# Kernel tuning notes

Hardware: AMD Instinct MI355X
Metric: run time of the kernel (lower is better)

The kernel has to match this reference:

```python
import jax, jax.numpy as jnp
import numpy as np

N_NODES = 100000
N_EDGES = 1600000
N_GRAPHS = 1000
D_IN = 128
HID = 128
OUT = 6


def setup_inputs() -> dict:
    key = jax.random.key(0)
    ks = jax.random.split(key, 12)
    s = 1.0 / np.sqrt(HID)
    x = jax.random.normal(ks[0], (N_NODES, D_IN), dtype=jnp.float32)
    ei = jax.random.randint(ks[1], (2, N_EDGES), 0, N_NODES, dtype=jnp.int64)
    batch = jnp.sort(jax.random.randint(ks[2], (N_NODES,), 0, N_GRAPHS, dtype=jnp.int64))
    return {
        "x": x,
        "ei": ei,
        "batch": batch,
        "W1a": jax.random.normal(ks[3], (D_IN, HID), dtype=jnp.float32) * s,
        "b1a": jnp.zeros((HID,), jnp.float32),
        "W1b": jax.random.normal(ks[4], (HID, HID), dtype=jnp.float32) * s,
        "b1b": jnp.zeros((HID,), jnp.float32),
        "W2a": jax.random.normal(ks[5], (HID, HID), dtype=jnp.float32) * s,
        "b2a": jnp.zeros((HID,), jnp.float32),
        "W2b": jax.random.normal(ks[6], (HID, HID), dtype=jnp.float32) * s,
        "b2b": jnp.zeros((HID,), jnp.float32),
        "Wlin": jax.random.normal(ks[7], (HID, OUT), dtype=jnp.float32) * s,
        "blin": jnp.zeros((OUT,), jnp.float32),
    }


def _gin_conv(x, src, dst, Wa, ba, Wb, bb):
    # PyG GINConv (eps=0): mlp(x_i + sum_{j->i} x_j)
    agg = jax.ops.segment_sum(x[src], dst, num_segments=N_NODES)
    h = agg + x
    h = jnp.maximum(h @ Wa + ba, 0.0)
    return h @ Wb + bb


def reference(x, ei, batch, W1a, b1a, W1b, b1b, W2a, b2a, W2b, b2b, Wlin, blin):
    src, dst = ei[0], ei[1]
    h = jnp.maximum(_gin_conv(x, src, dst, W1a, b1a, W1b, b1b), 0.0)
    # dropout is identity in eval mode
    h = _gin_conv(h, src, dst, W2a, b2a, W2b, b2b)
    # global mean pool per graph
    sums = jax.ops.segment_sum(h, batch, num_segments=N_GRAPHS)
    cnts = jax.ops.segment_sum(jnp.ones((h.shape[0], 1), h.dtype), batch, num_segments=N_GRAPHS)
    pooled = sums / jnp.maximum(cnts, 1.0)
    return pooled @ Wlin + blin
```

## Files before the change

kernel.cpp:

```cpp
#include <hip/hip_runtime.h>

#define N_NODES 100000
#define N_EDGES 1600000
#define N_GRAPHS 1000
#define HID 128
#define OUTD 6

#define BUCK_LOG 7
#define BUCK_W (1 << BUCK_LOG)
#define NBUCK ((N_NODES + BUCK_W - 1) >> BUCK_LOG)
#define BCAP 4096
#define FILL_BLOCKS 512
#define FILL_CHUNK 3128

#define CVT_BLOCKS 6250
#define GST_BLOCKS 391
#define PACK_BLOCKS 32
#define PREP_BLOCKS (CVT_BLOCKS + GST_BLOCKS + PACK_BLOCKS + FILL_BLOCKS)

typedef _Float16 h2 __attribute__((ext_vector_type(2)));
typedef _Float16 half8 __attribute__((ext_vector_type(8)));
typedef float f32x4 __attribute__((ext_vector_type(4)));

__global__ __launch_bounds__(256) void k_prep(const float* __restrict__ x,
                                              const int* __restrict__ batch,
                                              const int* __restrict__ srcv,
                                              const int* __restrict__ dstv,
                                              const float* __restrict__ W1a,
                                              const float* __restrict__ W1b,
                                              const float* __restrict__ W2a,
                                              const float* __restrict__ W2b,
                                              _Float16* __restrict__ X16,
                                              int* __restrict__ gstart,
                                              _Float16* __restrict__ P,
                                              int* __restrict__ bcur0,
                                              int* __restrict__ packed) {
    __shared__ int h[NBUCK];
    __shared__ int lcur[NBUCK];
    int b = blockIdx.x, t = threadIdx.x;
    if (b < FILL_BLOCKS) {
        int e0 = b * FILL_CHUNK;
        int e1 = min(e0 + FILL_CHUNK, N_EDGES);
        for (int i = t; i < NBUCK; i += 256) h[i] = 0;
        __syncthreads();
        int ev = e0 + ((e1 - e0) & ~3);
        for (int e = e0 + t * 4; e < ev; e += 1024) {
            int4 d4 = *(const int4*)(dstv + e);
            atomicAdd(&h[d4.x >> BUCK_LOG], 1);
            atomicAdd(&h[d4.y >> BUCK_LOG], 1);
            atomicAdd(&h[d4.z >> BUCK_LOG], 1);
            atomicAdd(&h[d4.w >> BUCK_LOG], 1);
        }
        for (int e = ev + t; e < e1; e += 256) atomicAdd(&h[dstv[e] >> BUCK_LOG], 1);
        __syncthreads();
        for (int i = t; i < NBUCK; i += 256) {
            int c = h[i];
            lcur[i] = c ? atomicAdd(&bcur0[i], c) : 0;
        }
        __syncthreads();
        for (int e = e0 + t * 4; e < ev; e += 1024) {
            int4 d4 = *(const int4*)(dstv + e);
            int4 s4 = *(const int4*)(srcv + e);
            int b0 = d4.x >> BUCK_LOG, b1 = d4.y >> BUCK_LOG;
            int b2 = d4.z >> BUCK_LOG, b3 = d4.w >> BUCK_LOG;
            int p0 = atomicAdd(&lcur[b0], 1);
            int p1 = atomicAdd(&lcur[b1], 1);
            int p2 = atomicAdd(&lcur[b2], 1);
            int p3 = atomicAdd(&lcur[b3], 1);
            if (p0 < BCAP) packed[b0 * BCAP + p0] = ((d4.x & (BUCK_W - 1)) << 20) | s4.x;
            if (p1 < BCAP) packed[b1 * BCAP + p1] = ((d4.y & (BUCK_W - 1)) << 20) | s4.y;
            if (p2 < BCAP) packed[b2 * BCAP + p2] = ((d4.z & (BUCK_W - 1)) << 20) | s4.z;
            if (p3 < BCAP) packed[b3 * BCAP + p3] = ((d4.w & (BUCK_W - 1)) << 20) | s4.w;
        }
        for (int e = ev + t; e < e1; e += 256) {
            int d = dstv[e];
            int bk = d >> BUCK_LOG;
            int pos = atomicAdd(&lcur[bk], 1);
            if (pos < BCAP) packed[bk * BCAP + pos] = ((d & (BUCK_W - 1)) << 20) | srcv[e];
        }
    } else if (b < FILL_BLOCKS + CVT_BLOCKS) {
        size_t i = ((size_t)(b - FILL_BLOCKS) * 256 + t) * 8;
        float4 v0 = *(const float4*)(x + i);
        float4 v1 = *(const float4*)(x + i + 4);
        half8 o;
        o[0] = (_Float16)v0.x; o[1] = (_Float16)v0.y; o[2] = (_Float16)v0.z; o[3] = (_Float16)v0.w;
        o[4] = (_Float16)v1.x; o[5] = (_Float16)v1.y; o[6] = (_Float16)v1.z; o[7] = (_Float16)v1.w;
        *(half8*)(X16 + i) = o;
    } else if (b < FILL_BLOCKS + CVT_BLOCKS + GST_BLOCKS) {
        int n = (b - FILL_BLOCKS - CVT_BLOCKS) * 256 + t;
        if (n < N_NODES) {
            int bb = batch[n];
            int prev = (n == 0) ? -1 : batch[n - 1];
            for (int g = prev + 1; g <= bb; ++g) gstart[g] = n;
            if (n == N_NODES - 1)
                for (int g = bb + 1; g <= N_GRAPHS; ++g) gstart[g] = N_NODES;
        }
    } else {
        int gid = (b - FILL_BLOCKS - CVT_BLOCKS - GST_BLOCKS) * 256 + t;
        int mat = gid >> 11;
        int r = gid & 2047;
        int ctks = r >> 6;
        int lane = r & 63;
        int col = (ctks >> 2) * 16 + (lane & 15);
        int k0 = (ctks & 3) * 32 + (lane >> 4) * 8;
        const float* W = (mat == 0) ? W1a : (mat == 1) ? W1b : (mat == 2) ? W2a : W2b;
        _Float16* dp = P + mat * 16384 + r * 8;
#pragma unroll
        for (int j = 0; j < 8; ++j) dp[j] = (_Float16)W[(k0 + j) * HID + col];
    }
}

__global__ __launch_bounds__(256) void k_csrfine(const int* __restrict__ packed,
                                                 const int* __restrict__ bcur0,
                                                 int* __restrict__ offsets,
                                                 int* __restrict__ csr_src) {
    __shared__ int hist[BUCK_W];
    __shared__ int scan[BUCK_W];
    __shared__ int cur[BUCK_W];
    __shared__ int red[4];
    int b = blockIdx.x;
    int base = b << BUCK_LOG;
    int t = threadIdx.x;
    int partial = 0;
    for (int j = t; j < b; j += 256) partial += bcur0[j];
#pragma unroll
    for (int d = 32; d > 0; d >>= 1) partial += __shfl_down(partial, d, 64);
    if ((t & 63) == 0) red[t >> 6] = partial;
    __syncthreads();
    int s = red[0] + red[1] + red[2] + red[3];
    int cnt = bcur0[b];
    const int* pb = packed + b * BCAP;

    if (t < BUCK_W) hist[t] = 0;
    __syncthreads();
    for (int i = t; i < cnt; i += 256) atomicAdd(&hist[pb[i] >> 20], 1);
    __syncthreads();
    if (t < BUCK_W) scan[t] = hist[t];
    __syncthreads();
    for (int d = 1; d < BUCK_W; d <<= 1) {
        int a = 0;
        if (t >= d && t < BUCK_W) a = scan[t - d];
        __syncthreads();
        if (t < BUCK_W) scan[t] += a;
        __syncthreads();
    }
    if (t < BUCK_W) {
        int node = base + t;
        if (node < N_NODES) {
            int excl = scan[t] - hist[t];
            offsets[node] = s + excl;
            cur[t] = excl;
        }
    }
    if (b == 0 && t == 0) offsets[N_NODES] = N_EDGES;
    __syncthreads();
    for (int i = t; i < cnt; i += 256) {
        int v = pb[i];
        int ln = v >> 20;
        int pos = atomicAdd(&cur[ln], 1);
        csr_src[s + pos] = v & 0xFFFFF;
    }
}

static __device__ __forceinline__ half8 shfl_xor_h8(half8 v, int mask) {
    union { half8 h; int i[4]; } a, b;
    a.h = v;
#pragma unroll
    for (int k = 0; k < 4; ++k) b.i[k] = __shfl_xor(a.i[k], mask, 64);
    return b.h;
}

__global__ __launch_bounds__(256) void k_gather16(const _Float16* __restrict__ x,
                                                  const int* __restrict__ csr,
                                                  const int* __restrict__ offs,
                                                  _Float16* __restrict__ out) {
    int t = threadIdx.x;
    int wave = t >> 6, lane = t & 63;
    int g = lane >> 4;
    int l = lane & 15;
    int node = __builtin_amdgcn_readfirstlane(blockIdx.x * 4 + wave);
    const half8* xp8 = (const half8*)x;
    int s = offs[node], e = offs[node + 1];

    half8 z = {0, 0, 0, 0, 0, 0, 0, 0};
    half8 acc0 = (g == 0) ? xp8[(size_t)node * 16 + l] : z;
    half8 acc1 = z;

    for (int base = s; base < e; base += 64) {
        int cnt = e - base;
        if (cnt > 64) cnt = 64;
        int myidx = (base + lane < e) ? csr[base + lane] : 0;
        int j = 0;
        for (; j + 16 <= cnt; j += 16) {
            int i0 = __shfl(myidx, j + g, 64);
            int i1 = __shfl(myidx, j + 4 + g, 64);
            int i2 = __shfl(myidx, j + 8 + g, 64);
            int i3 = __shfl(myidx, j + 12 + g, 64);
            acc0 += xp8[(size_t)i0 * 16 + l];
            acc1 += xp8[(size_t)i1 * 16 + l];
            acc0 += xp8[(size_t)i2 * 16 + l];
            acc1 += xp8[(size_t)i3 * 16 + l];
        }
        for (; j < cnt; j += 4) {
            int sl = j + g;
            int idx = __shfl(myidx, sl < cnt ? sl : 0, 64);
            if (sl < cnt) acc0 += xp8[(size_t)idx * 16 + l];
        }
    }
    half8 r = acc0 + acc1;
    r += shfl_xor_h8(r, 16);
    r += shfl_xor_h8(r, 32);
    if (g == 0) ((half8*)out)[(size_t)node * 16 + l] = r;
}

static __device__ __forceinline__ unsigned long long pack4(float v0, float v1,
                                                           float v2, float v3) {
    union { h2 h[2]; unsigned long long u; } u;
    h2 p0, p1;
    p0[0] = (_Float16)v0; p0[1] = (_Float16)v1;
    p1[0] = (_Float16)v2; p1[1] = (_Float16)v3;
    u.h[0] = p0; u.h[1] = p1;
    return u.u;
}

template <int RELU_OUT>
__global__ __launch_bounds__(256, 2) void k_mlp16(const _Float16* __restrict__ in,
                                                  const _Float16* __restrict__ Wap,
                                                  const float* __restrict__ ba,
                                                  const _Float16* __restrict__ Wbp,
                                                  const float* __restrict__ bb,
                                                  _Float16* __restrict__ out) {
    __shared__ uint4 WaS4[2048];
    __shared__ uint4 WbS4[2048];
    __shared__ unsigned long long hS[4][512];
    int t = threadIdx.x;
    int wave = t >> 6, lane = t & 63;
    int l = lane & 15, w = lane >> 4;
    int row0 = blockIdx.x * 256 + wave * 64;

    const uint4* wa4 = (const uint4*)Wap;
    const uint4* wb4 = (const uint4*)Wbp;
#pragma unroll
    for (int i = 0; i < 8; ++i) WaS4[t + i * 256] = wa4[t + i * 256];
#pragma unroll
    for (int i = 0; i < 8; ++i) WbS4[t + i * 256] = wb4[t + i * 256];
    __syncthreads();
    const half8* waf = (const half8*)WaS4;
    const half8* wbf = (const half8*)WbS4;
    unsigned long long* h64 = hS[wave];
    int swz = ((l & 3) << 2) ^ (((l >> 2) & 1) << 1);

    float4 baR[8], bbR[8];
#pragma unroll
    for (int ct = 0; ct < 8; ++ct) {
        baR[ct] = *(const float4*)(ba + ct * 16 + w * 4);
        bbR[ct] = *(const float4*)(bb + ct * 16 + w * 4);
    }

#pragma unroll
    for (int tile = 0; tile < 4; ++tile) {
        int row = row0 + tile * 16 + l;
        bool rok = row < N_NODES;
        const _Float16* rp = in + (size_t)row * HID + w * 8;
        half8 xf[4];
#pragma unroll
        for (int ks = 0; ks < 4; ++ks) {
            half8 v = {0, 0, 0, 0, 0, 0, 0, 0};
            if (rok) v = *(const half8*)(rp + ks * 32);
            xf[ks] = v;
        }
#pragma unroll
        for (int ct = 0; ct < 8; ++ct) {
            f32x4 c = {0.f, 0.f, 0.f, 0.f};
#pragma unroll
            for (int ks = 0; ks < 4; ++ks)
                c = __builtin_amdgcn_mfma_f32_16x16x32_f16(waf[(ct * 4 + ks) * 64 + lane],
                                                           xf[ks], c, 0, 0, 0);
            float4 b4 = baR[ct];
            h64[l * 32 + ((ct * 4 + w) ^ swz)] =
                pack4(fmaxf(c[0] + b4.x, 0.f), fmaxf(c[1] + b4.y, 0.f),
                      fmaxf(c[2] + b4.z, 0.f), fmaxf(c[3] + b4.w, 0.f));
        }
        half8 hf[4];
#pragma unroll
        for (int ks = 0; ks < 4; ++ks) {
            int slot = (ks * 8 + w * 2) ^ swz;
            hf[ks] = *(const half8*)&h64[l * 32 + slot];
        }
#pragma unroll
        for (int ct = 0; ct < 8; ++ct) {
            f32x4 c = {0.f, 0.f, 0.f, 0.f};
#pragma unroll
            for (int ks = 0; ks < 4; ++ks)
                c = __builtin_amdgcn_mfma_f32_16x16x32_f16(wbf[(ct * 4 + ks) * 64 + lane],
                                                           hf[ks], c, 0, 0, 0);
            float4 b4 = bbR[ct];
            float v0 = c[0] + b4.x, v1 = c[1] + b4.y, v2 = c[2] + b4.z, v3 = c[3] + b4.w;
            if (RELU_OUT) {
                v0 = fmaxf(v0, 0.f); v1 = fmaxf(v1, 0.f);
                v2 = fmaxf(v2, 0.f); v3 = fmaxf(v3, 0.f);
            }
            if (rok)
                *(unsigned long long*)(out + (size_t)row * HID + ct * 16 + w * 4) =
                    pack4(v0, v1, v2, v3);
        }
    }
}

__global__ __launch_bounds__(256) void k_pool_head(const _Float16* __restrict__ h,
                                                   const int* __restrict__ gstart,
                                                   const float* __restrict__ Wlin,
                                                   const float* __restrict__ blin,
                                                   float* __restrict__ out) {
    __shared__ float sums[4][HID];
    int g = blockIdx.x;
    int t = threadIdx.x;
    int wave = t >> 6, lane = t & 63;
    int s = gstart[g], e = gstart[g + 1];
    float ax = 0.f, ay = 0.f;
    const h2* hp = (const h2*)h;
    int r = s + wave;
    for (; r + 12 < e; r += 16) {
        h2 v0 = hp[(size_t)r * 64 + lane];
        h2 v1 = hp[(size_t)(r + 4) * 64 + lane];
        h2 v2 = hp[(size_t)(r + 8) * 64 + lane];
        h2 v3 = hp[(size_t)(r + 12) * 64 + lane];
        ax += (float)v0[0] + (float)v1[0] + (float)v2[0] + (float)v3[0];
        ay += (float)v0[1] + (float)v1[1] + (float)v2[1] + (float)v3[1];
    }
    for (; r < e; r += 4) {
        h2 v = hp[(size_t)r * 64 + lane];
        ax += (float)v[0];
        ay += (float)v[1];
    }
    sums[wave][2 * lane] = ax;
    sums[wave][2 * lane + 1] = ay;
    __syncthreads();
    if (wave != 0) return;
    float c = fmaxf((float)(e - s), 1.0f);
    float px = (sums[0][2 * lane] + sums[1][2 * lane] + sums[2][2 * lane] + sums[3][2 * lane]) / c;
    float py = (sums[0][2 * lane + 1] + sums[1][2 * lane + 1] + sums[2][2 * lane + 1] +
                sums[3][2 * lane + 1]) / c;
#pragma unroll
    for (int o = 0; o < OUTD; ++o) {
        float v = px * Wlin[(2 * lane) * OUTD + o] + py * Wlin[(2 * lane + 1) * OUTD + o];
#pragma unroll
        for (int d = 32; d > 0; d >>= 1) v += __shfl_down(v, d, 64);
        if (lane == 0) out[g * OUTD + o] = v + blin[o];
    }
}

extern "C" void kernel_launch(void* const* d_in, const int* in_sizes, int n_in,
                              void* d_out, int out_size, void* d_ws, size_t ws_size,
                              hipStream_t stream) {
    const float* x    = (const float*)d_in[0];
    const int*   ei   = (const int*)d_in[1];
    const int*   batch= (const int*)d_in[2];
    const float* W1a  = (const float*)d_in[3];
    const float* b1a  = (const float*)d_in[4];
    const float* W1b  = (const float*)d_in[5];
    const float* b1b  = (const float*)d_in[6];
    const float* W2a  = (const float*)d_in[7];
    const float* b2a  = (const float*)d_in[8];
    const float* W2b  = (const float*)d_in[9];
    const float* b2b  = (const float*)d_in[10];
    const float* Wlin = (const float*)d_in[11];
    const float* blin = (const float*)d_in[12];
    const int* src = ei;
    const int* dst = ei + N_EDGES;
    float* out = (float*)d_out;

    char* ws = (char*)d_ws;
    size_t off = 0;
    auto alloc = [&](size_t bytes) -> void* {
        void* p = ws + off;
        off += (bytes + 255) & ~(size_t)255;
        return p;
    };
    _Float16* X16 = (_Float16*)alloc(2ull * N_NODES * HID);
    _Float16* M   = (_Float16*)alloc(2ull * N_NODES * HID + 65536);
    _Float16* H1  = (_Float16*)alloc(2ull * N_NODES * HID + 65536);
    int*   csr_src = (int*)alloc(sizeof(int) * (size_t)N_EDGES);
    int*   offsets = (int*)alloc(sizeof(int) * (N_NODES + 1));
    int*   gstart  = (int*)alloc(sizeof(int) * (N_GRAPHS + 1));
    int*   bcur0   = (int*)alloc(sizeof(int) * NBUCK);
    _Float16* Wpack = (_Float16*)alloc(2ull * 4 * 16384);
    int* packed = (int*)H1;
    _Float16* M2 = M;
    _Float16* H2 = X16;
    (void)ws_size; (void)in_sizes; (void)n_in; (void)out_size;

    hipMemsetAsync(bcur0, 0, sizeof(int) * NBUCK, stream);

    k_prep<<<PREP_BLOCKS, 256, 0, stream>>>(x, batch, src, dst, W1a, W1b, W2a, W2b,
                                            X16, gstart, Wpack, bcur0, packed);
    k_csrfine<<<NBUCK, 256, 0, stream>>>(packed, bcur0, offsets, csr_src);

    k_gather16<<<N_NODES / 4, 256, 0, stream>>>(X16, csr_src, offsets, M);
    k_mlp16<1><<<(N_NODES + 255) / 256, 256, 0, stream>>>(M, Wpack + 0 * 16384, b1a,
                                                          Wpack + 1 * 16384, b1b, H1);
    k_gather16<<<N_NODES / 4, 256, 0, stream>>>(H1, csr_src, offsets, M2);
    k_mlp16<0><<<(N_NODES + 255) / 256, 256, 0, stream>>>(M2, Wpack + 2 * 16384, b2a,
                                                          Wpack + 3 * 16384, b2b, H2);

    k_pool_head<<<N_GRAPHS, 256, 0, stream>>>(H2, gstart, Wlin, blin, out);
}
```

Baseline: 312.6 us.

## Build CSR via per-node degree atomics and direct global scatter instead of bucketing

The two-pass bucket sort (pack edges into per-bucket staging, then a fine per-bucket histogram and scatter) is replaced by per-node degree counting with global atomics during prep, a per-bucket scan into offsets and cursors, and a separate scatter kernel that places each source by atomically incrementing its destination's cursor. This removes the packed staging buffer, the per-bucket capacity limit and the in-shared-memory fine sort. In exchange it issues 1.6M global atomics twice to random addresses, adds a kernel launch, and makes the within-node edge order nondeterministic.

After: 462.1 us. 47.8% more time.

```diff
diff --git a/kernel.cpp b/kernel.cpp
--- a/kernel.cpp
+++ b/kernel.cpp
@@ -9,7 +9,6 @@
 #define BUCK_LOG 7
 #define BUCK_W (1 << BUCK_LOG)
 #define NBUCK ((N_NODES + BUCK_W - 1) >> BUCK_LOG)
-#define BCAP 4096
 #define FILL_BLOCKS 512
 #define FILL_CHUNK 3128
 
@@ -34,9 +33,8 @@
                                               int* __restrict__ gstart,
                                               _Float16* __restrict__ P,
                                               int* __restrict__ bcur0,
-                                              int* __restrict__ packed) {
+                                              int* __restrict__ deg) {
     __shared__ int h[NBUCK];
-    __shared__ int lcur[NBUCK];
     int b = blockIdx.x, t = threadIdx.x;
     if (b < FILL_BLOCKS) {
         int e0 = b * FILL_CHUNK;
@@ -50,33 +48,20 @@
             atomicAdd(&h[d4.y >> BUCK_LOG], 1);
             atomicAdd(&h[d4.z >> BUCK_LOG], 1);
             atomicAdd(&h[d4.w >> BUCK_LOG], 1);
-        }
-        for (int e = ev + t; e < e1; e += 256) atomicAdd(&h[dstv[e] >> BUCK_LOG], 1);
+            atomicAdd(&deg[d4.x], 1);
+            atomicAdd(&deg[d4.y], 1);
+            atomicAdd(&deg[d4.z], 1);
+            atomicAdd(&deg[d4.w], 1);
+        }
+        for (int e = ev + t; e < e1; e += 256) {
+            int d = dstv[e];
+            atomicAdd(&h[d >> BUCK_LOG], 1);
+            atomicAdd(&deg[d], 1);
+        }
         __syncthreads();
         for (int i = t; i < NBUCK; i += 256) {
             int c = h[i];
-            lcur[i] = c ? atomicAdd(&bcur0[i], c) : 0;
-        }
-        __syncthreads();
-        for (int e = e0 + t * 4; e < ev; e += 1024) {
-            int4 d4 = *(const int4*)(dstv + e);
-            int4 s4 = *(const int4*)(srcv + e);
-            int b0 = d4.x >> BUCK_LOG, b1 = d4.y >> BUCK_LOG;
-            int b2 = d4.z >> BUCK_LOG, b3 = d4.w >> BUCK_LOG;
-            int p0 = atomicAdd(&lcur[b0], 1);
-            int p1 = atomicAdd(&lcur[b1], 1);
-            int p2 = atomicAdd(&lcur[b2], 1);
-            int p3 = atomicAdd(&lcur[b3], 1);
-            if (p0 < BCAP) packed[b0 * BCAP + p0] = ((d4.x & (BUCK_W - 1)) << 20) | s4.x;
-            if (p1 < BCAP) packed[b1 * BCAP + p1] = ((d4.y & (BUCK_W - 1)) << 20) | s4.y;
-            if (p2 < BCAP) packed[b2 * BCAP + p2] = ((d4.z & (BUCK_W - 1)) << 20) | s4.z;
-            if (p3 < BCAP) packed[b3 * BCAP + p3] = ((d4.w & (BUCK_W - 1)) << 20) | s4.w;
-        }
-        for (int e = ev + t; e < e1; e += 256) {
-            int d = dstv[e];
-            int bk = d >> BUCK_LOG;
-            int pos = atomicAdd(&lcur[bk], 1);
-            if (pos < BCAP) packed[bk * BCAP + pos] = ((d & (BUCK_W - 1)) << 20) | srcv[e];
+            if (c) atomicAdd(&bcur0[i], c);
         }
     } else if (b < FILL_BLOCKS + CVT_BLOCKS) {
         size_t i = ((size_t)(b - FILL_BLOCKS) * 256 + t) * 8;
@@ -110,13 +95,11 @@
     }
 }
 
-__global__ __launch_bounds__(256) void k_csrfine(const int* __restrict__ packed,
-                                                 const int* __restrict__ bcur0,
-                                                 int* __restrict__ offsets,
-                                                 int* __restrict__ csr_src) {
-    __shared__ int hist[BUCK_W];
-    __shared__ int scan[BUCK_W];
-    __shared__ int cur[BUCK_W];
+__global__ __launch_bounds__(256) void k_scan(const int* __restrict__ bcur0,
+                                              const int* __restrict__ deg,
+                                              int* __restrict__ offsets,
+                                              int* __restrict__ cursor) {
+    __shared__ int sc[BUCK_W];
     __shared__ int red[4];
     int b = blockIdx.x;
     int base = b << BUCK_LOG;
@@ -128,37 +111,51 @@
     if ((t & 63) == 0) red[t >> 6] = partial;
     __syncthreads();
     int s = red[0] + red[1] + red[2] + red[3];
-    int cnt = bcur0[b];
-    const int* pb = packed + b * BCAP;
-
-    if (t < BUCK_W) hist[t] = 0;
+    int node = base + t;
+    int d0 = 0;
+    if (t < BUCK_W) {
+        d0 = (node < N_NODES) ? deg[node] : 0;
+        sc[t] = d0;
+    }
     __syncthreads();
-    for (int i = t; i < cnt; i += 256) atomicAdd(&hist[pb[i] >> 20], 1);
-    __syncthreads();
-    if (t < BUCK_W) scan[t] = hist[t];
-    __syncthreads();
-    for (int d = 1; d < BUCK_W; d <<= 1) {
+    for (int dd = 1; dd < BUCK_W; dd <<= 1) {
         int a = 0;
-        if (t >= d && t < BUCK_W) a = scan[t - d];
+        if (t >= dd && t < BUCK_W) a = sc[t - dd];
         __syncthreads();
-        if (t < BUCK_W) scan[t] += a;
+        if (t < BUCK_W) sc[t] += a;
         __syncthreads();
     }
-    if (t < BUCK_W) {
-        int node = base + t;
-        if (node < N_NODES) {
-            int excl = scan[t] - hist[t];
-            offsets[node] = s + excl;
-            cur[t] = excl;
-        }
+    if (t < BUCK_W && node < N_NODES) {
+        int excl = sc[t] - d0;
+        offsets[node] = s + excl;
+        cursor[node] = s + excl;
     }
     if (b == 0 && t == 0) offsets[N_NODES] = N_EDGES;
-    __syncthreads();
-    for (int i = t; i < cnt; i += 256) {
-        int v = pb[i];
-        int ln = v >> 20;
-        int pos = atomicAdd(&cur[ln], 1);
-        csr_src[s + pos] = v & 0xFFFFF;
+}
+
+__global__ __launch_bounds__(256) void k_scatter(const int* __restrict__ srcv,
+                                                 const int* __restrict__ dstv,
+                                                 int* __restrict__ cursor,
+                                                 int* __restrict__ csr_src) {
+    int b = blockIdx.x, t = threadIdx.x;
+    int e0 = b * FILL_CHUNK;
+    int e1 = min(e0 + FILL_CHUNK, N_EDGES);
+    int ev = e0 + ((e1 - e0) & ~3);
+    for (int e = e0 + t * 4; e < ev; e += 1024) {
+        int4 d4 = *(const int4*)(dstv + e);
+        int4 s4 = *(const int4*)(srcv + e);
+        int p0 = atomicAdd(&cursor[d4.x], 1);
+        int p1 = atomicAdd(&cursor[d4.y], 1);
+        int p2 = atomicAdd(&cursor[d4.z], 1);
+        int p3 = atomicAdd(&cursor[d4.w], 1);
+        csr_src[p0] = s4.x;
+        csr_src[p1] = s4.y;
+        csr_src[p2] = s4.z;
+        csr_src[p3] = s4.w;
+    }
+    for (int e = ev + t; e < e1; e += 256) {
+        int p = atomicAdd(&cursor[dstv[e]], 1);
+        csr_src[p] = srcv[e];
     }
 }
 
@@ -383,18 +380,21 @@
     int*   csr_src = (int*)alloc(sizeof(int) * (size_t)N_EDGES);
     int*   offsets = (int*)alloc(sizeof(int) * (N_NODES + 1));
     int*   gstart  = (int*)alloc(sizeof(int) * (N_GRAPHS + 1));
-    int*   bcur0   = (int*)alloc(sizeof(int) * NBUCK);
+    int*   zeroed  = (int*)alloc(sizeof(int) * (NBUCK + N_NODES + 64));
+    int*   bcur0   = zeroed;
+    int*   deg     = zeroed + NBUCK;
+    int*   cursor  = (int*)alloc(sizeof(int) * (N_NODES + 64));
     _Float16* Wpack = (_Float16*)alloc(2ull * 4 * 16384);
-    int* packed = (int*)H1;
     _Float16* M2 = M;
     _Float16* H2 = X16;
     (void)ws_size; (void)in_sizes; (void)n_in; (void)out_size;
 
-    hipMemsetAsync(bcur0, 0, sizeof(int) * NBUCK, stream);
+    hipMemsetAsync(zeroed, 0, sizeof(int) * (NBUCK + N_NODES + 64), stream);
 
     k_prep<<<PREP_BLOCKS, 256, 0, stream>>>(x, batch, src, dst, W1a, W1b, W2a, W2b,
-                                            X16, gstart, Wpack, bcur0, packed);
-    k_csrfine<<<NBUCK, 256, 0, stream>>>(packed, bcur0, offsets, csr_src);
+                                            X16, gstart, Wpack, bcur0, deg);
+    k_scan<<<NBUCK, 256, 0, stream>>>(bcur0, deg, offsets, cursor);
+    k_scatter<<<FILL_BLOCKS, 256, 0, stream>>>(src, dst, cursor, csr_src);
 
     k_gather16<<<N_NODES / 4, 256, 0, stream>>>(X16, csr_src, offsets, M);
     k_mlp16<1><<<(N_NODES + 255) / 256, 256, 0, stream>>>(M, Wpack + 0 * 16384, b1a,
```
